# Performance work log

Measured on AMD Instinct MI355X. Metric: run time of the kernel, lower is better.

Reference implementation:

```python
import jax, jax.numpy as jnp
from jax import lax
import numpy as np

B, T, H, H2 = 2048, 512, 64, 16


def setup_inputs() -> dict:
    key = jax.random.key(0)
    ks = jax.random.split(key, 10)
    s_ih = 1.0 / np.sqrt(1 + 4 * H)   # xavier-ish scale for W_ih [4H, 1]
    s_hh = 1.0 / np.sqrt(H)
    return {
        "x":     jax.random.normal(ks[0], (B, T, 1), dtype=jnp.float32),
        "W_ih":  jax.random.normal(ks[1], (4 * H, 1), dtype=jnp.float32) * s_ih,
        "W_hh":  jax.random.normal(ks[2], (4 * H, H), dtype=jnp.float32) * s_hh,
        "b_ih":  jnp.zeros((4 * H,), dtype=jnp.float32),
        "b_hh":  jnp.zeros((4 * H,), dtype=jnp.float32),
        "fc1_w": jax.random.normal(ks[3], (H2, H), dtype=jnp.float32) * (1.0 / np.sqrt(H)),
        "fc1_b": jnp.zeros((H2,), dtype=jnp.float32),
        "fc2_w": jax.random.normal(ks[4], (1, H2), dtype=jnp.float32) * (1.0 / np.sqrt(H2)),
        "fc2_b": jnp.zeros((1,), dtype=jnp.float32),
    }


def _lstm_last_h(x, W_ih, W_hh, b_ih, b_hh):
    # PyTorch gate order: i, f, g, o. Precompute input projection for all steps.
    gx = jnp.einsum('bti,gi->btg', x, W_ih) + b_ih + b_hh  # [B, T, 4H]
    h0 = jnp.zeros((x.shape[0], W_hh.shape[1]), dtype=x.dtype)
    c0 = jnp.zeros_like(h0)

    def step(carry, g_t):
        h, c = carry
        g = g_t + h @ W_hh.T                       # [B, 4H]
        i, f, gc, o = jnp.split(g, 4, axis=-1)
        i = jax.nn.sigmoid(i)
        f = jax.nn.sigmoid(f)
        gc = jnp.tanh(gc)
        o = jax.nn.sigmoid(o)
        c = f * c + i * gc
        h = o * jnp.tanh(c)
        return (h, c), None

    (h, _), _ = lax.scan(step, (h0, c0), jnp.swapaxes(gx, 0, 1))  # scan over T
    return h  # [B, H] == out[:, -1, :]


def reference(x, W_ih, W_hh, b_ih, b_hh, fc1_w, fc1_b, fc2_w, fc2_b):
    h = _lstm_last_h(x, W_ih, W_hh, b_ih, b_hh)
    # dropout is identity in eval mode
    z = jax.nn.relu(h @ fc1_w.T + fc1_b)
    return z @ fc2_w.T + fc2_b  # [B, 1]
```

## Files before the change

### kernel.cpp

```cpp
#include <hip/hip_runtime.h>

namespace {

typedef __attribute__((ext_vector_type(8))) short short8;
typedef __attribute__((ext_vector_type(4))) float floatx4;

constexpr int T    = 512;
constexpr int H    = 64;
constexpr int TPB  = 512;
constexpr int MB   = 8;
constexpr int HST  = 136;
constexpr int XSTR = 516;
constexpr int FSTR = 68;

constexpr int DPP_ROR8 = 0x128;

__device__ __forceinline__ ushort f2bf(float x) {
  unsigned u = __float_as_uint(x);
  unsigned r = u + 0x7fffu + ((u >> 16) & 1u);
  return (ushort)(r >> 16);
}
__device__ __forceinline__ float bf2f(ushort h) {
  return __uint_as_float(((unsigned)h) << 16);
}
__device__ __forceinline__ float fsig(float x) {
  return __builtin_amdgcn_rcpf(1.0f + __expf(-x));
}
__device__ __forceinline__ float ftanh(float x) {
  return fmaf(-2.0f, __builtin_amdgcn_rcpf(1.0f + __expf(2.0f * x)), 1.0f);
}
__device__ __forceinline__ float swz8(float v) {
  return __int_as_float(__builtin_amdgcn_update_dpp(
      0, __float_as_int(v), DPP_ROR8, 0xf, 0xf, true));
}

__global__ __launch_bounds__(TPB, 2)
void lstm_mfma(const float* __restrict__ xg,
               const float* __restrict__ W_ih,
               const float* __restrict__ W_hh,
               const float* __restrict__ b_ih,
               const float* __restrict__ b_hh,
               const float* __restrict__ fc1_w,
               const float* __restrict__ fc1_b,
               const float* __restrict__ fc2_w,
               const float* __restrict__ fc2_b,
               float* __restrict__ out)
{
  __shared__ __align__(16) ushort hA[MB * HST];
  __shared__ __align__(16) ushort hB[MB * HST];
  __shared__ __align__(16) float  xs[MB * XSTR];
  __shared__ __align__(16) float  hf[MB * FSTR];
  __shared__ float zs[MB][16];

  const int tid  = threadIdx.x;
  const int b0   = blockIdx.x * MB;
  const int lane = tid & 63;
  const int wj   = tid >> 6;
  const int n    = lane & 15;
  const int kg   = lane >> 4;
  const int bat  = n & 7;
  const int nhi  = n >> 3;

  for (int i = tid; i < MB * T / 4; i += TPB) {
    const int xb = i >> 7, tq = i & 127;
    float4 v = ((const float4*)(xg + (size_t)(b0 + xb) * T))[tq];
    *(float4*)&xs[xb * XSTR + tq * 4] = v;
  }
  for (int i = tid; i < MB * HST; i += TPB) { hA[i] = 0; hB[i] = 0; }

  short8 whi[2][2], wlo[2][2];
#pragma unroll
  for (int tt = 0; tt < 2; ++tt) {
    const int r    = 2 * wj + tt;
    const int arow = 64 * (n & 3) + 4 * r + (n >> 2);
    const float* wr = W_hh + arow * H + 8 * kg;
    const float4 p0 = *(const float4*)(wr + 0);
    const float4 p1 = *(const float4*)(wr + 4);
    const float4 p2 = *(const float4*)(wr + 32);
    const float4 p3 = *(const float4*)(wr + 36);
    const float v0[8] = {p0.x, p0.y, p0.z, p0.w, p1.x, p1.y, p1.z, p1.w};
    const float v1[8] = {p2.x, p2.y, p2.z, p2.w, p3.x, p3.y, p3.z, p3.w};
#pragma unroll
    for (int j = 0; j < 8; ++j) {
      const ushort h0 = f2bf(v0[j]);
      whi[tt][0][j] = (short)h0;
      wlo[tt][0][j] = (short)f2bf(v0[j] - bf2f(h0));
      const ushort h1 = f2bf(v1[j]);
      whi[tt][1][j] = (short)h1;
      wlo[tt][1][j] = (short)f2bf(v1[j] - bf2f(h1));
    }
  }

  const int u = 4 * (2 * wj + nhi) + kg;
  float bia[4], wih[4];
#pragma unroll
  for (int j = 0; j < 4; ++j) {
    const int row = 64 * j + u;
    bia[j] = b_ih[row] + b_hh[row];
    wih[j] = W_ih[row];
  }

  const int rdoff = bat * HST + nhi * 64 + 8 * kg;
  const int woff  = bat * HST + u;
  const float* xq = &xs[bat * XSTR];
  float c = 0.0f, hk = 0.0f;

  __syncthreads();

#define STEP(HR, HW, TT)                                                       \
  {                                                                            \
    const ushort* hb = (HR) + rdoff;                                           \
    const short8 f0 = *(const short8*)(hb + 0);       \
    const short8 f1 = *(const short8*)(hb + 32);                 \
    const floatx4 zf = {0.f, 0.f, 0.f, 0.f};                                   \
    floatx4 d1 = __builtin_amdgcn_mfma_f32_16x16x32_bf16(whi[0][0], f0, zf, 0, 0, 0); \
    floatx4 d2 = __builtin_amdgcn_mfma_f32_16x16x32_bf16(wlo[0][0], f0, zf, 0, 0, 0); \
    floatx4 e1 = __builtin_amdgcn_mfma_f32_16x16x32_bf16(whi[1][0], f0, zf, 0, 0, 0); \
    floatx4 e2 = __builtin_amdgcn_mfma_f32_16x16x32_bf16(wlo[1][0], f0, zf, 0, 0, 0); \
    d1 = __builtin_amdgcn_mfma_f32_16x16x32_bf16(whi[0][1], f1, d1, 0, 0, 0);  \
    d2 = __builtin_amdgcn_mfma_f32_16x16x32_bf16(wlo[0][1], f1, d2, 0, 0, 0);  \
    e1 = __builtin_amdgcn_mfma_f32_16x16x32_bf16(whi[1][1], f1, e1, 0, 0, 0);  \
    e2 = __builtin_amdgcn_mfma_f32_16x16x32_bf16(wlo[1][1], f1, e2, 0, 0, 0);  \
    const float xt = xq[(TT)];                                                 \
    float p[4];                                                                \
    _Pragma("unroll") for (int j = 0; j < 4; ++j) {                            \
      const float sA = d1[j] + d2[j];                  \
      const float sB = e1[j] + e2[j];                  \
      const float pA = sA + swz8(sA);               \
      const float pB = sB + swz8(sB);                                          \
      p[j] = (nhi ? pB : pA) + fmaf(xt, wih[j], bia[j]);                       \
    }                                                                          \
    const float ig = fsig(p[0]);                                               \
    const float fg = fsig(p[1]);                                               \
    const float gc = ftanh(p[2]);                                              \
    const float og = fsig(p[3]);                                               \
    c  = fmaf(fg, c, ig * gc);                                                 \
    hk = og * ftanh(c);                                                        \
    const ushort hib = f2bf(hk);                                               \
    ushort* hw = (HW) + woff;                                                  \
    hw[0]  = hib;                                                              \
    hw[64] = f2bf(hk - bf2f(hib));                                             \
    __syncthreads();                                                           \
  }

  for (int t = 0; t < T; t += 2) {
    STEP(hA, hB, t);
    STEP(hB, hA, t + 1);
  }
#undef STEP

  hf[bat * FSTR + u] = hk;
  __syncthreads();
  if (tid < MB * 16) {
    const int bq = tid >> 4, j2 = tid & 15;
    float s = fc1_b[j2];
    const float* fw = fc1_w + j2 * H;
#pragma unroll
    for (int k = 0; k < H; ++k) s = fmaf(hf[bq * FSTR + k], fw[k], s);
    s = fmaxf(s, 0.0f);
    zs[bq][j2] = s * fc2_w[j2];
  }
  __syncthreads();
  if (tid < MB) {
    float s = fc2_b[0];
#pragma unroll
    for (int j = 0; j < 16; ++j) s += zs[tid][j];
    out[b0 + tid] = s;
  }
}

}

extern "C" void kernel_launch(void* const* d_in, const int* in_sizes, int n_in,
                              void* d_out, int out_size, void* d_ws, size_t ws_size,
                              hipStream_t stream) {
  const float* xg    = (const float*)d_in[0];
  const float* W_ih  = (const float*)d_in[1];
  const float* W_hh  = (const float*)d_in[2];
  const float* b_ih  = (const float*)d_in[3];
  const float* b_hh  = (const float*)d_in[4];
  const float* fc1_w = (const float*)d_in[5];
  const float* fc1_b = (const float*)d_in[6];
  const float* fc2_w = (const float*)d_in[7];
  const float* fc2_b = (const float*)d_in[8];
  float* out = (float*)d_out;

  dim3 grid(2048 / MB);
  dim3 block(TPB);
  hipLaunchKernelGGL(lstm_mfma, grid, block, 0, stream,
                     xg, W_ih, W_hh, b_ih, b_hh, fc1_w, fc1_b, fc2_w, fc2_b, out);
}
```

Baseline: 298.2 us.

## Halve batch per block to 4 and widen each wave to four gate tiles

The block shrinks to 256 threads handling 4 batch rows. Each wave now computes four 16-row gate tiles with 16 MFMAs per step, and the hi/lo bf16 halves of h are laid out as separate B-matrix columns, so the per-step cross-lane reduction uses a select plus one DPP swizzle. The grid doubles so more blocks spread across CUs, and barrier cost per block falls with fewer waves. The hi part of h is now made by truncation instead of rounding, with the residual still stored as lo. The risk is twice as much MFMA work per wave on the serial recurrence path, with half the batch throughput per MFMA.

```diff
diff --git a/kernel.cpp b/kernel.cpp
--- a/kernel.cpp
+++ b/kernel.cpp
@@ -7,9 +7,9 @@
 
 constexpr int T    = 512;
 constexpr int H    = 64;
-constexpr int TPB  = 512;
-constexpr int MB   = 8;
-constexpr int HST  = 136;
+constexpr int TPB  = 256;
+constexpr int MB   = 4;
+constexpr int HST  = 72;
 constexpr int XSTR = 516;
 constexpr int FSTR = 68;
 
@@ -46,8 +46,8 @@
                const float* __restrict__ fc2_b,
                float* __restrict__ out)
 {
-  __shared__ __align__(16) ushort hA[MB * HST];
-  __shared__ __align__(16) ushort hB[MB * HST];
+  __shared__ __align__(16) ushort hA[8 * HST];
+  __shared__ __align__(16) ushort hB[8 * HST];
   __shared__ __align__(16) float  xs[MB * XSTR];
   __shared__ __align__(16) float  hf[MB * FSTR];
   __shared__ float zs[MB][16];
@@ -58,21 +58,23 @@
   const int wj   = tid >> 6;
   const int n    = lane & 15;
   const int kg   = lane >> 4;
-  const int bat  = n & 7;
-  const int nhi  = n >> 3;
+  const int bat  = n & 3;
+  const int q    = n >> 2;
+  const bool q1  = (q & 1) != 0;
+  const bool q2  = (q & 2) != 0;
 
   for (int i = tid; i < MB * T / 4; i += TPB) {
     const int xb = i >> 7, tq = i & 127;
     float4 v = ((const float4*)(xg + (size_t)(b0 + xb) * T))[tq];
     *(float4*)&xs[xb * XSTR + tq * 4] = v;
   }
-  for (int i = tid; i < MB * HST; i += TPB) { hA[i] = 0; hB[i] = 0; }
-
-  short8 whi[2][2], wlo[2][2];
-#pragma unroll
-  for (int tt = 0; tt < 2; ++tt) {
-    const int r    = 2 * wj + tt;
-    const int arow = 64 * (n & 3) + 4 * r + (n >> 2);
+  for (int i = tid; i < 8 * HST; i += TPB) { hA[i] = 0; hB[i] = 0; }
+
+  short8 whi[4][2], wlo[4][2];
+#pragma unroll
+  for (int tt = 0; tt < 4; ++tt) {
+    const int gt   = 4 * wj + tt;
+    const int arow = 64 * (n & 3) + 4 * gt + (n >> 2);
     const float* wr = W_hh + arow * H + 8 * kg;
     const float4 p0 = *(const float4*)(wr + 0);
     const float4 p1 = *(const float4*)(wr + 4);
@@ -91,7 +93,7 @@
     }
   }
 
-  const int u = 4 * (2 * wj + nhi) + kg;
+  const int u = 16 * wj + 4 * q + kg;
   float bia[4], wih[4];
 #pragma unroll
   for (int j = 0; j < 4; ++j) {
@@ -100,8 +102,9 @@
     wih[j] = W_ih[row];
   }
 
-  const int rdoff = bat * HST + nhi * 64 + 8 * kg;
-  const int woff  = bat * HST + u;
+  const int rdoff = (2 * bat + (q >> 1)) * HST + 8 * kg;
+  const int whi_o = (2 * bat + 0) * HST + u;
+  const int wlo_o = (2 * bat + 1) * HST + u;
   const float* xq = &xs[bat * XSTR];
   float c = 0.0f, hk = 0.0f;
 
@@ -110,25 +113,33 @@
 #define STEP(HR, HW, TT)                                                       \
   {                                                                            \
     const ushort* hb = (HR) + rdoff;                                           \
-    const short8 f0 = *(const short8*)(hb + 0);       \
+    const short8 f0 = *(const short8*)(hb + 0);        \
     const short8 f1 = *(const short8*)(hb + 32);                 \
     const floatx4 zf = {0.f, 0.f, 0.f, 0.f};                                   \
-    floatx4 d1 = __builtin_amdgcn_mfma_f32_16x16x32_bf16(whi[0][0], f0, zf, 0, 0, 0); \
-    floatx4 d2 = __builtin_amdgcn_mfma_f32_16x16x32_bf16(wlo[0][0], f0, zf, 0, 0, 0); \
-    floatx4 e1 = __builtin_amdgcn_mfma_f32_16x16x32_bf16(whi[1][0], f0, zf, 0, 0, 0); \
-    floatx4 e2 = __builtin_amdgcn_mfma_f32_16x16x32_bf16(wlo[1][0], f0, zf, 0, 0, 0); \
-    d1 = __builtin_amdgcn_mfma_f32_16x16x32_bf16(whi[0][1], f1, d1, 0, 0, 0);  \
-    d2 = __builtin_amdgcn_mfma_f32_16x16x32_bf16(wlo[0][1], f1, d2, 0, 0, 0);  \
-    e1 = __builtin_amdgcn_mfma_f32_16x16x32_bf16(whi[1][1], f1, e1, 0, 0, 0);  \
-    e2 = __builtin_amdgcn_mfma_f32_16x16x32_bf16(wlo[1][1], f1, e2, 0, 0, 0);  \
+    floatx4 d1[4], d2[4];                                                      \
+    _Pragma("unroll") for (int tt = 0; tt < 4; ++tt) {                         \
+      d1[tt] = __builtin_amdgcn_mfma_f32_16x16x32_bf16(whi[tt][0], f0, zf, 0, 0, 0); \
+      d2[tt] = __builtin_amdgcn_mfma_f32_16x16x32_bf16(wlo[tt][0], f0, zf, 0, 0, 0); \
+    }                                                                          \
+    _Pragma("unroll") for (int tt = 0; tt < 4; ++tt) {                         \
+      d1[tt] = __builtin_amdgcn_mfma_f32_16x16x32_bf16(whi[tt][1], f1, d1[tt], 0, 0, 0); \
+      d2[tt] = __builtin_amdgcn_mfma_f32_16x16x32_bf16(wlo[tt][1], f1, d2[tt], 0, 0, 0); \
+    }                                                                          \
     const float xt = xq[(TT)];                                                 \
+    float pinit[4];                                                            \
+    _Pragma("unroll") for (int j = 0; j < 4; ++j)                              \
+      pinit[j] = fmaf(xt, wih[j], bia[j]);                                     \
     float p[4];                                                                \
     _Pragma("unroll") for (int j = 0; j < 4; ++j) {                            \
-      const float sA = d1[j] + d2[j];                  \
-      const float sB = e1[j] + e2[j];                  \
-      const float pA = sA + swz8(sA);               \
-      const float pB = sB + swz8(sB);                                          \
-      p[j] = (nhi ? pB : pA) + fmaf(xt, wih[j], bia[j]);                       \
+      const float s0 = d1[0][j] + d2[0][j];                                    \
+      const float s1 = d1[1][j] + d2[1][j];                                    \
+      const float s2 = d1[2][j] + d2[2][j];                                    \
+      const float s3 = d1[3][j] + d2[3][j];                                    \
+      const float tl = q1 ? s1 : s0;                                           \
+      const float th = q1 ? s3 : s2;                                           \
+      const float own = q2 ? th : tl;                                          \
+      const float snd = q2 ? tl : th;         \
+      p[j] = own + swz8(snd) + pinit[j];                                       \
     }                                                                          \
     const float ig = fsig(p[0]);                                               \
     const float fg = fsig(p[1]);                                               \
@@ -136,10 +147,9 @@
     const float og = fsig(p[3]);                                               \
     c  = fmaf(fg, c, ig * gc);                                                 \
     hk = og * ftanh(c);                                                        \
-    const ushort hib = f2bf(hk);                                               \
-    ushort* hw = (HW) + woff;                                                  \
-    hw[0]  = hib;                                                              \
-    hw[64] = f2bf(hk - bf2f(hib));                                             \
+    const ushort hib = (ushort)(__float_as_uint(hk) >> 16);   \
+    (HW)[whi_o] = hib;                                                         \
+    (HW)[wlo_o] = f2bf(hk - bf2f(hib));       \
     __syncthreads();                                                           \
   }
 
```

Measured after the change: 326.5 us. 1.09x slower.

## Double block to 1024 threads, one gate tile per wave, split hi/lo rows

Applied to the files above, without the earlier changes.

Each block now uses 16 waves instead of 8. Each wave computes a single 16-row gate tile with 4 MFMAs per step instead of two tiles with 8, which halves the per-wave serial dependency chain in each recurrent step. The hidden-state buffer is reorganised so the hi and lo bf16 halves of h sit in separate rows. The nhi lane half now writes the lo residual, and the hi part is taken by truncation instead of rounding. Occupancy drops to one block per CU, and the per-step barrier now spans 16 waves, which adds synchronisation cost.

```diff
diff --git a/kernel.cpp b/kernel.cpp
--- a/kernel.cpp
+++ b/kernel.cpp
@@ -5,13 +5,14 @@
 typedef __attribute__((ext_vector_type(8))) short short8;
 typedef __attribute__((ext_vector_type(4))) float floatx4;
 
-constexpr int T    = 512;
-constexpr int H    = 64;
-constexpr int TPB  = 512;
-constexpr int MB   = 8;
-constexpr int HST  = 136;
-constexpr int XSTR = 516;
-constexpr int FSTR = 68;
+constexpr int T     = 512;
+constexpr int H     = 64;
+constexpr int TPB   = 1024;
+constexpr int MB    = 8;
+constexpr int HST   = 72;
+constexpr int HROWS = 16;
+constexpr int XSTR  = 516;
+constexpr int FSTR  = 68;
 
 constexpr int DPP_ROR8 = 0x128;
 
@@ -34,7 +35,7 @@
       0, __float_as_int(v), DPP_ROR8, 0xf, 0xf, true));
 }
 
-__global__ __launch_bounds__(TPB, 2)
+__global__ __launch_bounds__(TPB, 1)
 void lstm_mfma(const float* __restrict__ xg,
                const float* __restrict__ W_ih,
                const float* __restrict__ W_hh,
@@ -46,8 +47,8 @@
                const float* __restrict__ fc2_b,
                float* __restrict__ out)
 {
-  __shared__ __align__(16) ushort hA[MB * HST];
-  __shared__ __align__(16) ushort hB[MB * HST];
+  __shared__ __align__(16) ushort hA[HROWS * HST];
+  __shared__ __align__(16) ushort hB[HROWS * HST];
   __shared__ __align__(16) float  xs[MB * XSTR];
   __shared__ __align__(16) float  hf[MB * FSTR];
   __shared__ float zs[MB][16];
@@ -66,13 +67,11 @@
     float4 v = ((const float4*)(xg + (size_t)(b0 + xb) * T))[tq];
     *(float4*)&xs[xb * XSTR + tq * 4] = v;
   }
-  for (int i = tid; i < MB * HST; i += TPB) { hA[i] = 0; hB[i] = 0; }
+  for (int i = tid; i < HROWS * HST; i += TPB) { hA[i] = 0; hB[i] = 0; }
 
-  short8 whi[2][2], wlo[2][2];
-#pragma unroll
-  for (int tt = 0; tt < 2; ++tt) {
-    const int r    = 2 * wj + tt;
-    const int arow = 64 * (n & 3) + 4 * r + (n >> 2);
+  short8 whi[2], wlo[2];
+  {
+    const int arow = 64 * (n & 3) + 4 * wj + (n >> 2);
     const float* wr = W_hh + arow * H + 8 * kg;
     const float4 p0 = *(const float4*)(wr + 0);
     const float4 p1 = *(const float4*)(wr + 4);
@@ -83,15 +82,15 @@
 #pragma unroll
     for (int j = 0; j < 8; ++j) {
       const ushort h0 = f2bf(v0[j]);
-      whi[tt][0][j] = (short)h0;
-      wlo[tt][0][j] = (short)f2bf(v0[j] - bf2f(h0));
+      whi[0][j] = (short)h0;
+      wlo[0][j] = (short)f2bf(v0[j] - bf2f(h0));
       const ushort h1 = f2bf(v1[j]);
-      whi[tt][1][j] = (short)h1;
-      wlo[tt][1][j] = (short)f2bf(v1[j] - bf2f(h1));
+      whi[1][j] = (short)h1;
+      wlo[1][j] = (short)f2bf(v1[j] - bf2f(h1));
     }
   }
 
-  const int u = 4 * (2 * wj + nhi) + kg;
+  const int u = 4 * wj + kg;
   float bia[4], wih[4];
 #pragma unroll
   for (int j = 0; j < 4; ++j) {
@@ -100,8 +99,8 @@
     wih[j] = W_ih[row];
   }
 
-  const int rdoff = bat * HST + nhi * 64 + 8 * kg;
-  const int woff  = bat * HST + u;
+  const int rdoff = (2 * bat + nhi) * HST + 8 * kg;
+  const int woff  = (2 * bat + nhi) * HST + u;
   const float* xq = &xs[bat * XSTR];
   float c = 0.0f, hk = 0.0f;
 
@@ -110,25 +109,18 @@
 #define STEP(HR, HW, TT)                                                       \
   {                                                                            \
     const ushort* hb = (HR) + rdoff;                                           \
-    const short8 f0 = *(const short8*)(hb + 0);       \
-    const short8 f1 = *(const short8*)(hb + 32);                 \
+    const short8 f0 = *(const short8*)(hb + 0);     \
+    const short8 f1 = *(const short8*)(hb + 32);             \
     const floatx4 zf = {0.f, 0.f, 0.f, 0.f};                                   \
-    floatx4 d1 = __builtin_amdgcn_mfma_f32_16x16x32_bf16(whi[0][0], f0, zf, 0, 0, 0); \
-    floatx4 d2 = __builtin_amdgcn_mfma_f32_16x16x32_bf16(wlo[0][0], f0, zf, 0, 0, 0); \
-    floatx4 e1 = __builtin_amdgcn_mfma_f32_16x16x32_bf16(whi[1][0], f0, zf, 0, 0, 0); \
-    floatx4 e2 = __builtin_amdgcn_mfma_f32_16x16x32_bf16(wlo[1][0], f0, zf, 0, 0, 0); \
-    d1 = __builtin_amdgcn_mfma_f32_16x16x32_bf16(whi[0][1], f1, d1, 0, 0, 0);  \
-    d2 = __builtin_amdgcn_mfma_f32_16x16x32_bf16(wlo[0][1], f1, d2, 0, 0, 0);  \
-    e1 = __builtin_amdgcn_mfma_f32_16x16x32_bf16(whi[1][1], f1, e1, 0, 0, 0);  \
-    e2 = __builtin_amdgcn_mfma_f32_16x16x32_bf16(wlo[1][1], f1, e2, 0, 0, 0);  \
+    floatx4 d1 = __builtin_amdgcn_mfma_f32_16x16x32_bf16(whi[0], f0, zf, 0, 0, 0); \
+    floatx4 d2 = __builtin_amdgcn_mfma_f32_16x16x32_bf16(wlo[0], f0, zf, 0, 0, 0); \
+    d1 = __builtin_amdgcn_mfma_f32_16x16x32_bf16(whi[1], f1, d1, 0, 0, 0);     \
+    d2 = __builtin_amdgcn_mfma_f32_16x16x32_bf16(wlo[1], f1, d2, 0, 0, 0);     \
     const float xt = xq[(TT)];                                                 \
     float p[4];                                                                \
     _Pragma("unroll") for (int j = 0; j < 4; ++j) {                            \
-      const float sA = d1[j] + d2[j];                  \
-      const float sB = e1[j] + e2[j];                  \
-      const float pA = sA + swz8(sA);               \
-      const float pB = sB + swz8(sB);                                          \
-      p[j] = (nhi ? pB : pA) + fmaf(xt, wih[j], bia[j]);                       \
+      const float s = d1[j] + d2[j];                                           \
+      p[j] = s + swz8(s) + fmaf(xt, wih[j], bia[j]);                           \
     }                                                                          \
     const float ig = fsig(p[0]);                                               \
     const float fg = fsig(p[1]);                                               \
@@ -136,10 +128,8 @@
     const float og = fsig(p[3]);                                               \
     c  = fmaf(fg, c, ig * gc);                                                 \
     hk = og * ftanh(c);                                                        \
-    const ushort hib = f2bf(hk);                                               \
-    ushort* hw = (HW) + woff;                                                  \
-    hw[0]  = hib;                                                              \
-    hw[64] = f2bf(hk - bf2f(hib));                                             \
+    const ushort hib = (ushort)(__float_as_uint(hk) >> 16);   \
+    (HW)[woff] = nhi ? f2bf(hk - bf2f(hib)) : hib;                             \
     __syncthreads();                                                           \
   }
 
@@ -149,7 +139,7 @@
   }
 #undef STEP
 
-  hf[bat * FSTR + u] = hk;
+  if (nhi == 0) hf[bat * FSTR + u] = hk;
   __syncthreads();
   if (tid < MB * 16) {
     const int bq = tid >> 4, j2 = tid & 15;
```

Result: slower. 353.7 us (+18.6%).
